# Kernel tuning notes

Hardware: AMD Instinct MI355X
Metric: run time of the kernel (lower is better)

## Reference

```python
import jax, jax.numpy as jnp
import numpy as np

N_NODES = 100000
N_EDGES = 800000
F_IN, HID, N_CLS = 256, 128, 32


def setup_inputs() -> dict:
    key = jax.random.key(0)
    k1, k2, k3, k4, k5 = jax.random.split(key, 5)
    features = jax.random.normal(k1, (N_NODES, F_IN), dtype=jnp.float32)
    # random directed edges with no self loops (so add_remaining_self_loops == append all loops)
    src = jax.random.randint(k2, (N_EDGES,), 0, N_NODES)
    off = jax.random.randint(k3, (N_EDGES,), 1, N_NODES)
    dst = (src + off) % N_NODES
    edge_index = jnp.stack([src, dst]).astype(jnp.int64)
    # Glorot-style params for the two GCNConv layers
    W1 = jax.random.normal(k4, (F_IN, HID), dtype=jnp.float32) * (1.0 / np.sqrt(F_IN))
    b1 = jnp.zeros((HID,), dtype=jnp.float32)
    W2 = jax.random.normal(k5, (HID, N_CLS), dtype=jnp.float32) * (1.0 / np.sqrt(HID))
    b2 = jnp.zeros((N_CLS,), dtype=jnp.float32)
    return {"features": features, "edge_index": edge_index, "W1": W1, "b1": b1, "W2": W2, "b2": b2}


def _gcn_conv(x, W, b, src, dst, norm, n):
    xw = x @ W                                  # [N, d_out] dense GEMM
    msg = xw[src] * norm[:, None]               # gather + scale, [E, d_out]
    out = jax.ops.segment_sum(msg, dst, num_segments=n)  # scatter-add to targets
    return out + b


def reference(features, edge_index, W1, b1, W2, b2):
    n = features.shape[0]
    # add_remaining_self_loops (input has none, so append all)
    loops = jnp.arange(n, dtype=edge_index.dtype)
    src = jnp.concatenate([edge_index[0], loops])
    dst = jnp.concatenate([edge_index[1], loops])
    # gcn_norm: deg over targets, sym normalization deg^-1/2 A deg^-1/2
    deg = jax.ops.segment_sum(jnp.ones_like(src, dtype=features.dtype), dst, num_segments=n)
    dinv = jnp.where(deg > 0, jax.lax.rsqrt(deg), 0.0)
    norm = dinv[src] * dinv[dst]
    x = _gcn_conv(features, W1, b1, src, dst, norm, n)
    x = jax.nn.relu(x)
    # dropout is identity at inference (training=False)
    x = _gcn_conv(x, W2, b2, src, dst, norm, n)
    return jax.nn.log_softmax(x, axis=1)
```

## Files before the change

### kernel.cpp

```cpp
#include <hip/hip_runtime.h>
#include <hip/hip_bf16.h>

typedef __bf16 bf16_t;
typedef __attribute__((ext_vector_type(8))) __bf16 bf16x8;
typedef __attribute__((ext_vector_type(4))) float f32x4;

__device__ inline void packB_one(const float* __restrict__ B, bf16_t* __restrict__ Bp,
                                 int N, int idx) {
    int j    = idx & 7;
    int lane = (idx >> 3) & 63;
    int st   = idx >> 9;
    int nt   = N >> 4;
    int s = st / nt, t = st - s * nt;
    int k = s * 32 + (lane >> 4) * 8 + j;
    int n = t * 16 + (lane & 15);
    Bp[idx] = (bf16_t)B[(size_t)k * N + n];
}

__global__ __launch_bounds__(256) void k_front(
        const float* __restrict__ feat, bf16_t* __restrict__ Ap,
        const float* __restrict__ W1, bf16_t* __restrict__ Bp1,
        const float* __restrict__ W2, bf16_t* __restrict__ Bp2,
        const int* __restrict__ dst, int* __restrict__ deg,
        int* __restrict__ rank, int apThreads, int E, int AB) {
    int b = blockIdx.x, t = threadIdx.x;
    if (b < AB) {
        int idx = b * 256 + t;
        if (idx >= apThreads) return;
        int w    = idx >> 6;
        int lane = idx & 63;
        int r16 = lane & 15, quad = lane >> 4;
        const float* arow = feat + (size_t)(w * 16 + r16) * 256 + quad * 8;
        bf16_t* opb = Ap + (size_t)w * 4096 + lane * 8;
#pragma unroll
        for (int s = 0; s < 8; ++s) {
            const float* ap = arow + s * 32;
            bf16x8 a;
#pragma unroll
            for (int j = 0; j < 8; ++j) a[j] = (bf16_t)ap[j];
            *(bf16x8*)(opb + s * 512) = a;
        }
        return;
    }
    b -= AB;
    const int PACK_BLOCKS = (32768 + 4096) / 256;
    if (b < PACK_BLOCKS) {
        int idx = b * 256 + t;
        if (idx < 32768) packB_one(W1, Bp1, 128, idx);
        else             packB_one(W2, Bp2, 32, idx - 32768);
        return;
    }
    int i = (b - PACK_BLOCKS) * 1024 + t * 4;
    if (i + 4 <= E) {
        int4 v = *(const int4*)(dst + i);
        int4 r;
        r.x = atomicAdd(&deg[v.x], 1);
        r.y = atomicAdd(&deg[v.y], 1);
        r.z = atomicAdd(&deg[v.z], 1);
        r.w = atomicAdd(&deg[v.w], 1);
        *(int4*)(rank + i) = r;
    } else {
        for (int j = 0; j < 4; ++j)
            if (i + j < E) rank[i + j] = atomicAdd(&deg[dst[i + j]], 1);
    }
}

__global__ __launch_bounds__(256) void k_dinv_scan1(const int* __restrict__ deg,
                                                    float* __restrict__ dinv,
                                                    int* __restrict__ bsum, int n) {
    __shared__ int red[256];
    int b = blockIdx.x, t = threadIdx.x;
    int base = b * 1024 + t * 4;
    int s = 0;
#pragma unroll
    for (int j = 0; j < 4; ++j) {
        int i = base + j;
        if (i < n) { int d = deg[i]; s += d; dinv[i] = rsqrtf((float)(d + 1)); }
    }
    red[t] = s;
    __syncthreads();
    for (int d = 128; d > 0; d >>= 1) {
        if (t < d) red[t] += red[t + d];
        __syncthreads();
    }
    if (t == 0) bsum[b] = red[0];
}

__global__ __launch_bounds__(256) void k_scan3f(const int* __restrict__ deg,
                                                const int* __restrict__ bsum, int nb,
                                                int* __restrict__ rowPtr, int n) {
    __shared__ int red[256];
    __shared__ int boff[256];
    int b = blockIdx.x, t = threadIdx.x;
    int base = b * 1024 + t * 4;
    int v[4]; int s = 0;
#pragma unroll
    for (int j = 0; j < 4; ++j) { int i = base + j; v[j] = (i < n) ? deg[i] : 0; s += v[j]; }
    red[t] = s;
    boff[t] = (t < nb) ? bsum[t] : 0;
    __syncthreads();
    for (int d = 1; d < 256; d <<= 1) {
        int u  = (t >= d) ? red[t - d]  : 0;
        int u2 = (t >= d) ? boff[t - d] : 0;
        __syncthreads();
        red[t] += u;
        boff[t] += u2;
        __syncthreads();
    }
    int blockOff = (b == 0) ? 0 : boff[b - 1];
    if (b == 0 && t == 0) rowPtr[n] = boff[nb - 1];
    int run = blockOff + red[t] - s;
#pragma unroll
    for (int j = 0; j < 4; ++j) {
        int i = base + j;
        if (i < n) { rowPtr[i] = run; run += v[j]; }
    }
}

template <int KSTEPS, int NTILES>
__global__ __launch_bounds__(256) void k_gemm_scatter(
        const bf16_t* __restrict__ Ap, const bf16_t* __restrict__ Bp,
        bf16_t* __restrict__ C, int M, int gemmBlocks,
        const int* __restrict__ src, const int* __restrict__ dst,
        const int* __restrict__ rank, const int* __restrict__ rowPtr,
        const float* __restrict__ dinv, int2* __restrict__ edata, int E) {
    int b = blockIdx.x, t = threadIdx.x;
    if (b < gemmBlocks) {
        int wave = (b * 256 + t) >> 6;
        if (wave * 16 >= M) return;
        int lane = t & 63;
        int r16 = lane & 15, quad = lane >> 4;
        const int N = NTILES * 16;
        f32x4 acc[NTILES] = {};
        const bf16_t* apb = Ap + (size_t)wave * (KSTEPS * 512) + lane * 8;
#pragma unroll
        for (int s = 0; s < KSTEPS; ++s) {
            bf16x8 a = *(const bf16x8*)(apb + s * 512);
            const bf16_t* bp = Bp + ((size_t)(s * NTILES) * 64 + lane) * 8;
#pragma unroll
            for (int tt = 0; tt < NTILES; ++tt) {
                bf16x8 bb = *(const bf16x8*)(bp + tt * 512);
                acc[tt] = __builtin_amdgcn_mfma_f32_16x16x32_bf16(a, bb, acc[tt], 0, 0, 0);
            }
        }
#pragma unroll
        for (int tt = 0; tt < NTILES; ++tt)
#pragma unroll
            for (int r = 0; r < 4; ++r)
                C[(size_t)(wave * 16 + quad * 4 + r) * N + tt * 16 + r16] = (bf16_t)acc[tt][r];
        return;
    }
    int i = (b - gemmBlocks) * 1024 + t * 4;
    if (i + 4 <= E) {
        int4 s4 = *(const int4*)(src + i);
        int4 d4 = *(const int4*)(dst + i);
        int4 r4 = *(const int4*)(rank + i);
        int p0 = rowPtr[d4.x] + r4.x, p1 = rowPtr[d4.y] + r4.y;
        int p2 = rowPtr[d4.z] + r4.z, p3 = rowPtr[d4.w] + r4.w;
        int2 e0; e0.x = s4.x; e0.y = __float_as_int(dinv[s4.x] * dinv[d4.x]);
        int2 e1; e1.x = s4.y; e1.y = __float_as_int(dinv[s4.y] * dinv[d4.y]);
        int2 e2; e2.x = s4.z; e2.y = __float_as_int(dinv[s4.z] * dinv[d4.z]);
        int2 e3; e3.x = s4.w; e3.y = __float_as_int(dinv[s4.w] * dinv[d4.w]);
        edata[p0] = e0; edata[p1] = e1; edata[p2] = e2; edata[p3] = e3;
    } else {
        for (int j = 0; j < 4; ++j) {
            int e = i + j;
            if (e >= E) break;
            int s = src[e], d = dst[e];
            int2 p; p.x = s; p.y = __float_as_int(dinv[s] * dinv[d]);
            edata[rowPtr[d] + rank[e]] = p;
        }
    }
}

template <int KSTEPS, int NTILES>
__global__ __launch_bounds__(256) void k_gemm_p(
        const bf16_t* __restrict__ Ap, const bf16_t* __restrict__ Bp,
        bf16_t* __restrict__ C, int M) {
    int wave = (blockIdx.x * blockDim.x + threadIdx.x) >> 6;
    if (wave * 16 >= M) return;
    int lane = threadIdx.x & 63;
    int r16 = lane & 15, quad = lane >> 4;
    const int N = NTILES * 16;
    f32x4 acc[NTILES] = {};
    const bf16_t* apb = Ap + (size_t)wave * (KSTEPS * 512) + lane * 8;
#pragma unroll
    for (int s = 0; s < KSTEPS; ++s) {
        bf16x8 a = *(const bf16x8*)(apb + s * 512);
        const bf16_t* bp = Bp + ((size_t)(s * NTILES) * 64 + lane) * 8;
#pragma unroll
        for (int t = 0; t < NTILES; ++t) {
            bf16x8 b = *(const bf16x8*)(bp + t * 512);
            acc[t] = __builtin_amdgcn_mfma_f32_16x16x32_bf16(a, b, acc[t], 0, 0, 0);
        }
    }
#pragma unroll
    for (int t = 0; t < NTILES; ++t)
#pragma unroll
        for (int r = 0; r < 4; ++r)
            C[(size_t)(wave * 16 + quad * 4 + r) * N + t * 16 + r16] = (bf16_t)acc[t][r];
}

__global__ __launch_bounds__(256) void k_agg1(
        const int* __restrict__ rowPtr, const int2* __restrict__ edata,
        const bf16_t* __restrict__ XW1, const float* __restrict__ dinv,
        const float* __restrict__ b1, bf16_t* __restrict__ Hp, int n) {
    int wave = (blockIdx.x * blockDim.x + threadIdx.x) >> 6;
    if (wave >= n) return;
    int lane = threadIdx.x & 63;
    int fl = (lane & 15) << 3;
    int h  = lane >> 4;
    int r0 = rowPtr[wave], r1 = rowPtr[wave + 1];
    float a0[8] = {}, a1[8] = {};
    int k = r0 + h;
    for (; k + 4 < r1; k += 8) {
        int2 e0 = edata[k], e1 = edata[k + 4];
        float w0 = __int_as_float(e0.y), w1 = __int_as_float(e1.y);
        bf16x8 x0 = *(const bf16x8*)(XW1 + ((size_t)e0.x << 7) + fl);
        bf16x8 x1 = *(const bf16x8*)(XW1 + ((size_t)e1.x << 7) + fl);
#pragma unroll
        for (int j = 0; j < 8; ++j) { a0[j] += (float)x0[j] * w0; a1[j] += (float)x1[j] * w1; }
    }
    if (k < r1) {
        int2 e0 = edata[k];
        float w0 = __int_as_float(e0.y);
        bf16x8 x0 = *(const bf16x8*)(XW1 + ((size_t)e0.x << 7) + fl);
#pragma unroll
        for (int j = 0; j < 8; ++j) a0[j] += (float)x0[j] * w0;
    }
#pragma unroll
    for (int j = 0; j < 8; ++j) {
        a0[j] += a1[j];
        a0[j] += __shfl_xor(a0[j], 16);
        a0[j] += __shfl_xor(a0[j], 32);
    }
    if (h == 0) {
        float d = dinv[wave], d2 = d * d;
        bf16x8 xs = *(const bf16x8*)(XW1 + ((size_t)wave << 7) + fl);
        bf16x8 hv;
#pragma unroll
        for (int j = 0; j < 8; ++j) {
            float v = a0[j] + (float)xs[j] * d2 + b1[fl + j];
            hv[j] = (bf16_t)fmaxf(v, 0.f);
        }
        int q = lane & 15;
        size_t off = (((size_t)(wave >> 4) * 4 + (q >> 2)) * 64
                      + (wave & 15) + 16 * (q & 3)) * 8;
        *(bf16x8*)(Hp + off) = hv;
    }
}

__global__ __launch_bounds__(256) void k_agg2(
        const int* __restrict__ rowPtr, const int2* __restrict__ edata,
        const bf16_t* __restrict__ XW2, const float* __restrict__ dinv,
        const float* __restrict__ b2, float* __restrict__ out, int n) {
    int wave = (blockIdx.x * blockDim.x + threadIdx.x) >> 6;
    if (wave >= n) return;
    int lane = threadIdx.x & 63;
    int g = lane & 15;
    int h = lane >> 4;
    int r0 = rowPtr[wave], r1 = rowPtr[wave + 1];
    float a00 = 0.f, a01 = 0.f, a10 = 0.f, a11 = 0.f;
    int k = r0 + h;
    for (; k + 4 < r1; k += 8) {
        int2 e0 = edata[k], e1 = edata[k + 4];
        float w0 = __int_as_float(e0.y), w1 = __int_as_float(e1.y);
        unsigned p0 = *(const unsigned*)(XW2 + ((size_t)e0.x << 5) + 2 * g);
        unsigned p1 = *(const unsigned*)(XW2 + ((size_t)e1.x << 5) + 2 * g);
        a00 += __int_as_float(p0 << 16) * w0;
        a01 += __int_as_float(p0 & 0xffff0000u) * w0;
        a10 += __int_as_float(p1 << 16) * w1;
        a11 += __int_as_float(p1 & 0xffff0000u) * w1;
    }
    if (k < r1) {
        int2 e0 = edata[k];
        float w0 = __int_as_float(e0.y);
        unsigned p0 = *(const unsigned*)(XW2 + ((size_t)e0.x << 5) + 2 * g);
        a00 += __int_as_float(p0 << 16) * w0;
        a01 += __int_as_float(p0 & 0xffff0000u) * w0;
    }
    float v0 = a00 + a10, v1 = a01 + a11;
    v0 += __shfl_xor(v0, 16); v0 += __shfl_xor(v0, 32);
    v1 += __shfl_xor(v1, 16); v1 += __shfl_xor(v1, 32);
    float d = dinv[wave], d2 = d * d;
    unsigned ps = *(const unsigned*)(XW2 + ((size_t)wave << 5) + 2 * g);
    float2 bb = *(const float2*)(b2 + 2 * g);
    v0 += __int_as_float(ps << 16) * d2 + bb.x;
    v1 += __int_as_float(ps & 0xffff0000u) * d2 + bb.y;
    float mx = fmaxf(v0, v1);
#pragma unroll
    for (int m = 8; m >= 1; m >>= 1) mx = fmaxf(mx, __shfl_xor(mx, m));
    float s = expf(v0 - mx) + expf(v1 - mx);
#pragma unroll
    for (int m = 8; m >= 1; m >>= 1) s += __shfl_xor(s, m);
    if (h == 0) {
        float ls = logf(s);
        float2 o; o.x = v0 - mx - ls; o.y = v1 - mx - ls;
        *(float2*)(out + ((size_t)wave << 5) + 2 * g) = o;
    }
}

extern "C" void kernel_launch(void* const* d_in, const int* in_sizes, int n_in,
                              void* d_out, int out_size, void* d_ws, size_t ws_size,
                              hipStream_t stream) {
    const float* feat = (const float*)d_in[0];
    const int*   eidx = (const int*)d_in[1];
    const float* W1   = (const float*)d_in[2];
    const float* b1   = (const float*)d_in[3];
    const float* W2   = (const float*)d_in[4];
    const float* b2   = (const float*)d_in[5];
    float* out = (float*)d_out;

    const int FIN = 256, HID = 128, NCLS = 32;
    const int N = in_sizes[0] / FIN;
    const int E = in_sizes[1] / 2;
    const int* src = eidx;
    const int* dst = eidx + E;

    char* ws = (char*)d_ws;
    size_t o = 0;
    auto alloc = [&](size_t bytes) -> void* {
        void* p = ws + o;
        o = (o + bytes + 255) & ~(size_t)255;
        return p;
    };
    int*    deg    = (int*)   alloc((size_t)N * 4);
    int*    rank   = (int*)   alloc((size_t)E * 4);
    float*  dinv   = (float*) alloc((size_t)N * 4);
    int*    rowPtr = (int*)   alloc((size_t)(N + 1) * 4);
    int*    bsum   = (int*)   alloc(256 * 4);
    bf16_t* Bp1    = (bf16_t*)alloc((size_t)(FIN / 32) * (HID / 16) * 512 * 2);
    bf16_t* Bp2    = (bf16_t*)alloc((size_t)(HID / 32) * (NCLS / 16) * 512 * 2);
    int2*   edata  = (int2*)  alloc((size_t)E * 8);
    bf16_t* Ap1    = (bf16_t*)alloc((size_t)N * FIN * 2);
    bf16_t* XW1    = (bf16_t*)alloc((size_t)N * HID * 2);
    bf16_t* Hp     = (bf16_t*)alloc((size_t)N * HID * 2);
    bf16_t* XW2    = XW1;

    const int T = 256;
    const int NB = (N + 1023) >> 10;
    const int apThreads = (N / 16) * 64;
    const int AB = (apThreads + T - 1) / T;
    const int PACK_BLOCKS = (32768 + 4096) / 256;
    const int DEG_BLOCKS  = (E + 1023) / 1024;
    hipMemsetAsync(deg, 0, (size_t)N * 4, stream);
    k_front<<<AB + PACK_BLOCKS + DEG_BLOCKS, T, 0, stream>>>(
        feat, Ap1, W1, Bp1, W2, Bp2, dst, deg, rank, apThreads, E, AB);
    k_dinv_scan1<<<NB, T, 0, stream>>>(deg, dinv, bsum, N);
    k_scan3f    <<<NB, T, 0, stream>>>(deg, bsum, NB, rowPtr, N);

    {
        int waves = (N + 15) / 16;
        int gemmBlocks = (waves * 64 + T - 1) / T;
        int scatBlocks = (E + 1023) / 1024;
        k_gemm_scatter<8, 8><<<gemmBlocks + scatBlocks, T, 0, stream>>>(
            Ap1, Bp1, XW1, N, gemmBlocks, src, dst, rank, rowPtr, dinv, edata, E);
    }
    k_agg1<<<(N * 64 + T - 1) / T, T, 0, stream>>>(rowPtr, edata, XW1, dinv, b1, Hp, N);

    {
        int waves = (N + 15) / 16;
        k_gemm_p<4, 2><<<(waves * 64 + T - 1) / T, T, 0, stream>>>(Hp, Bp2, XW2, N);
    }
    k_agg2<<<(N * 64 + T - 1) / T, T, 0, stream>>>(rowPtr, edata, XW2, dinv, b2, out, N);
}
```

Baseline: 333.1 us.

## Fuse fp32-to-bf16 feature conversion into layer-1 GEMM and reschedule front kernels

The layer-1 GEMM now reads fp32 features directly and converts them to bf16 in registers. This removes the separate packed-A buffer write and re-read of about 100k×256 elements. The GEMM moves into the front kernel alongside the degree-count atomics, weight packing becomes its own small launch before it, and edge scatter becomes a standalone kernel. The aggregation kernels hoist the self-loop loads ahead of their edge loops, and the log-softmax switches to fast __expf/__logf intrinsics. The cost is one extra launch, and the uncoalesced fp32 row reads in the GEMM may be less efficient than the old packed layout.

```diff
diff --git a/kernel.cpp b/kernel.cpp
--- a/kernel.cpp
+++ b/kernel.cpp
@@ -17,52 +17,64 @@
     Bp[idx] = (bf16_t)B[(size_t)k * N + n];
 }
 
+template <int KSTEPS, int NTILES>
 __global__ __launch_bounds__(256) void k_front(
-        const float* __restrict__ feat, bf16_t* __restrict__ Ap,
+        const float* __restrict__ feat, const bf16_t* __restrict__ Bp1r,
+        bf16_t* __restrict__ XW1, int M,
         const float* __restrict__ W1, bf16_t* __restrict__ Bp1,
         const float* __restrict__ W2, bf16_t* __restrict__ Bp2,
         const int* __restrict__ dst, int* __restrict__ deg,
-        int* __restrict__ rank, int apThreads, int E, int AB) {
+        int* __restrict__ rank, int E, int DEGB, int GEMMB) {
     int b = blockIdx.x, t = threadIdx.x;
-    if (b < AB) {
-        int idx = b * 256 + t;
-        if (idx >= apThreads) return;
-        int w    = idx >> 6;
-        int lane = idx & 63;
+    if (b < DEGB) {
+        int i = b * 1024 + t * 4;
+        if (i + 4 <= E) {
+            int4 v = *(const int4*)(dst + i);
+            int4 r;
+            r.x = atomicAdd(&deg[v.x], 1);
+            r.y = atomicAdd(&deg[v.y], 1);
+            r.z = atomicAdd(&deg[v.z], 1);
+            r.w = atomicAdd(&deg[v.w], 1);
+            *(int4*)(rank + i) = r;
+        } else {
+            for (int j = 0; j < 4; ++j)
+                if (i + j < E) rank[i + j] = atomicAdd(&deg[dst[i + j]], 1);
+        }
+        return;
+    }
+    b -= DEGB;
+    if (b < GEMMB) {
+        int wave = (b * 256 + t) >> 6;
+        if (wave * 16 >= M) return;
+        int lane = t & 63;
         int r16 = lane & 15, quad = lane >> 4;
-        const float* arow = feat + (size_t)(w * 16 + r16) * 256 + quad * 8;
-        bf16_t* opb = Ap + (size_t)w * 4096 + lane * 8;
-#pragma unroll
-        for (int s = 0; s < 8; ++s) {
+        const int K = KSTEPS * 32, N = NTILES * 16;
+        f32x4 acc[NTILES] = {};
+        const float* arow = feat + (size_t)(wave * 16 + r16) * K + quad * 8;
+#pragma unroll
+        for (int s = 0; s < KSTEPS; ++s) {
             const float* ap = arow + s * 32;
             bf16x8 a;
 #pragma unroll
             for (int j = 0; j < 8; ++j) a[j] = (bf16_t)ap[j];
-            *(bf16x8*)(opb + s * 512) = a;
-        }
+            const bf16_t* bp = Bp1r + ((size_t)(s * NTILES) * 64 + lane) * 8;
+#pragma unroll
+            for (int tt = 0; tt < NTILES; ++tt) {
+                bf16x8 bb = *(const bf16x8*)(bp + tt * 512);
+                acc[tt] = __builtin_amdgcn_mfma_f32_16x16x32_bf16(a, bb, acc[tt], 0, 0, 0);
+            }
+        }
+#pragma unroll
+        for (int tt = 0; tt < NTILES; ++tt)
+#pragma unroll
+            for (int r = 0; r < 4; ++r)
+                XW1[(size_t)(wave * 16 + quad * 4 + r) * N + tt * 16 + r16] = (bf16_t)acc[tt][r];
         return;
     }
-    b -= AB;
-    const int PACK_BLOCKS = (32768 + 4096) / 256;
-    if (b < PACK_BLOCKS) {
-        int idx = b * 256 + t;
-        if (idx < 32768) packB_one(W1, Bp1, 128, idx);
-        else             packB_one(W2, Bp2, 32, idx - 32768);
-        return;
-    }
-    int i = (b - PACK_BLOCKS) * 1024 + t * 4;
-    if (i + 4 <= E) {
-        int4 v = *(const int4*)(dst + i);
-        int4 r;
-        r.x = atomicAdd(&deg[v.x], 1);
-        r.y = atomicAdd(&deg[v.y], 1);
-        r.z = atomicAdd(&deg[v.z], 1);
-        r.w = atomicAdd(&deg[v.w], 1);
-        *(int4*)(rank + i) = r;
-    } else {
-        for (int j = 0; j < 4; ++j)
-            if (i + j < E) rank[i + j] = atomicAdd(&deg[dst[i + j]], 1);
-    }
+    b -= GEMMB;
+    int idx = b * 256 + t;
+    if (idx < 32768) packB_one(W1, Bp1, 128, idx);
+    else             packB_one(W2, Bp2, 32, idx - 32768);
 }
 
 __global__ __launch_bounds__(256) void k_dinv_scan1(const int* __restrict__ deg,
@@ -117,40 +129,11 @@
     }
 }
 
-template <int KSTEPS, int NTILES>
-__global__ __launch_bounds__(256) void k_gemm_scatter(
-        const bf16_t* __restrict__ Ap, const bf16_t* __restrict__ Bp,
-        bf16_t* __restrict__ C, int M, int gemmBlocks,
+__global__ __launch_bounds__(256) void k_scatter(
         const int* __restrict__ src, const int* __restrict__ dst,
         const int* __restrict__ rank, const int* __restrict__ rowPtr,
         const float* __restrict__ dinv, int2* __restrict__ edata, int E) {
-    int b = blockIdx.x, t = threadIdx.x;
-    if (b < gemmBlocks) {
-        int wave = (b * 256 + t) >> 6;
-        if (wave * 16 >= M) return;
-        int lane = t & 63;
-        int r16 = lane & 15, quad = lane >> 4;
-        const int N = NTILES * 16;
-        f32x4 acc[NTILES] = {};
-        const bf16_t* apb = Ap + (size_t)wave * (KSTEPS * 512) + lane * 8;
-#pragma unroll
-        for (int s = 0; s < KSTEPS; ++s) {
-            bf16x8 a = *(const bf16x8*)(apb + s * 512);
-            const bf16_t* bp = Bp + ((size_t)(s * NTILES) * 64 + lane) * 8;
-#pragma unroll
-            for (int tt = 0; tt < NTILES; ++tt) {
-                bf16x8 bb = *(const bf16x8*)(bp + tt * 512);
-                acc[tt] = __builtin_amdgcn_mfma_f32_16x16x32_bf16(a, bb, acc[tt], 0, 0, 0);
-            }
-        }
-#pragma unroll
-        for (int tt = 0; tt < NTILES; ++tt)
-#pragma unroll
-            for (int r = 0; r < 4; ++r)
-                C[(size_t)(wave * 16 + quad * 4 + r) * N + tt * 16 + r16] = (bf16_t)acc[tt][r];
-        return;
-    }
-    int i = (b - gemmBlocks) * 1024 + t * 4;
+    int i = (blockIdx.x * 256 + threadIdx.x) * 4;
     if (i + 4 <= E) {
         int4 s4 = *(const int4*)(src + i);
         int4 d4 = *(const int4*)(dst + i);
@@ -211,6 +194,8 @@
     int fl = (lane & 15) << 3;
     int h  = lane >> 4;
     int r0 = rowPtr[wave], r1 = rowPtr[wave + 1];
+    float d = dinv[wave], d2 = d * d;
+    bf16x8 xs = *(const bf16x8*)(XW1 + ((size_t)wave << 7) + fl);
     float a0[8] = {}, a1[8] = {};
     int k = r0 + h;
     for (; k + 4 < r1; k += 8) {
@@ -235,8 +220,6 @@
         a0[j] += __shfl_xor(a0[j], 32);
     }
     if (h == 0) {
-        float d = dinv[wave], d2 = d * d;
-        bf16x8 xs = *(const bf16x8*)(XW1 + ((size_t)wave << 7) + fl);
         bf16x8 hv;
 #pragma unroll
         for (int j = 0; j < 8; ++j) {
@@ -260,6 +243,9 @@
     int g = lane & 15;
     int h = lane >> 4;
     int r0 = rowPtr[wave], r1 = rowPtr[wave + 1];
+    float d = dinv[wave], d2 = d * d;
+    unsigned ps = *(const unsigned*)(XW2 + ((size_t)wave << 5) + 2 * g);
+    float2 bb = *(const float2*)(b2 + 2 * g);
     float a00 = 0.f, a01 = 0.f, a10 = 0.f, a11 = 0.f;
     int k = r0 + h;
     for (; k + 4 < r1; k += 8) {
@@ -282,19 +268,16 @@
     float v0 = a00 + a10, v1 = a01 + a11;
     v0 += __shfl_xor(v0, 16); v0 += __shfl_xor(v0, 32);
     v1 += __shfl_xor(v1, 16); v1 += __shfl_xor(v1, 32);
-    float d = dinv[wave], d2 = d * d;
-    unsigned ps = *(const unsigned*)(XW2 + ((size_t)wave << 5) + 2 * g);
-    float2 bb = *(const float2*)(b2 + 2 * g);
     v0 += __int_as_float(ps << 16) * d2 + bb.x;
     v1 += __int_as_float(ps & 0xffff0000u) * d2 + bb.y;
     float mx = fmaxf(v0, v1);
 #pragma unroll
     for (int m = 8; m >= 1; m >>= 1) mx = fmaxf(mx, __shfl_xor(mx, m));
-    float s = expf(v0 - mx) + expf(v1 - mx);
+    float s = __expf(v0 - mx) + __expf(v1 - mx);
 #pragma unroll
     for (int m = 8; m >= 1; m >>= 1) s += __shfl_xor(s, m);
     if (h == 0) {
-        float ls = logf(s);
+        float ls = __logf(s);
         float2 o; o.x = v0 - mx - ls; o.y = v1 - mx - ls;
         *(float2*)(out + ((size_t)wave << 5) + 2 * g) = o;
     }
@@ -332,32 +315,26 @@
     bf16_t* Bp1    = (bf16_t*)alloc((size_t)(FIN / 32) * (HID / 16) * 512 * 2);
     bf16_t* Bp2    = (bf16_t*)alloc((size_t)(HID / 32) * (NCLS / 16) * 512 * 2);
     int2*   edata  = (int2*)  alloc((size_t)E * 8);
-    bf16_t* Ap1    = (bf16_t*)alloc((size_t)N * FIN * 2);
     bf16_t* XW1    = (bf16_t*)alloc((size_t)N * HID * 2);
     bf16_t* Hp     = (bf16_t*)alloc((size_t)N * HID * 2);
     bf16_t* XW2    = XW1;
 
     const int T = 256;
     const int NB = (N + 1023) >> 10;
-    const int apThreads = (N / 16) * 64;
-    const int AB = (apThreads + T - 1) / T;
-    const int PACK_BLOCKS = (32768 + 4096) / 256;
-    const int DEG_BLOCKS  = (E + 1023) / 1024;
+    const int DEGB  = (E + 1023) / 1024;
+    const int GEMMB = (((N + 15) / 16) * 64 + T - 1) / T;
+    const int PACKB = (32768 + 4096) / 256;
     hipMemsetAsync(deg, 0, (size_t)N * 4, stream);
-    k_front<<<AB + PACK_BLOCKS + DEG_BLOCKS, T, 0, stream>>>(
-        feat, Ap1, W1, Bp1, W2, Bp2, dst, deg, rank, apThreads, E, AB);
+    {
+        k_front<8, 8><<<PACKB, T, 0, stream>>>(
+            feat, Bp1, XW1, 0, W1, Bp1, W2, Bp2, dst, deg, rank, 0, 0, 0);
+    }
+    k_front<8, 8><<<DEGB + GEMMB, T, 0, stream>>>(
+        feat, Bp1, XW1, N, W1, Bp1, W2, Bp2, dst, deg, rank, E, DEGB, GEMMB);
     k_dinv_scan1<<<NB, T, 0, stream>>>(deg, dinv, bsum, N);
     k_scan3f    <<<NB, T, 0, stream>>>(deg, bsum, NB, rowPtr, N);
-
-    {
-        int waves = (N + 15) / 16;
-        int gemmBlocks = (waves * 64 + T - 1) / T;
-        int scatBlocks = (E + 1023) / 1024;
-        k_gemm_scatter<8, 8><<<gemmBlocks + scatBlocks, T, 0, stream>>>(
-            Ap1, Bp1, XW1, N, gemmBlocks, src, dst, rank, rowPtr, dinv, edata, E);
-    }
+    k_scatter   <<<(E + 1023) / 1024, T, 0, stream>>>(src, dst, rank, rowPtr, dinv, edata, E);
     k_agg1<<<(N * 64 + T - 1) / T, T, 0, stream>>>(rowPtr, edata, XW1, dinv, b1, Hp, N);
-
     {
         int waves = (N + 15) / 16;
         k_gemm_p<4, 2><<<(waves * 64 + T - 1) / T, T, 0, stream>>>(Hp, Bp2, XW2, N);
```

Result: faster. 325.4 us (-2.3%).
